# Kernel optimization log

Measured on AMD Instinct MI355X. Metric: run time of the kernel, lower is better.

## Reference

```python
import jax, jax.numpy as jnp
import numpy as np

N = 100000  # nodes
E = 600000  # edges (avg degree ~6, mesh-like)
HID = 128


def _lin(key, fan_in, fan_out):
    # torch Linear default init: U(-1/sqrt(fan_in), 1/sqrt(fan_in))
    bound = 1.0 / np.sqrt(fan_in)
    return jax.random.uniform(key, (fan_in, fan_out), jnp.float32, -bound, bound)


def setup_inputs() -> dict:
    key = jax.random.key(0)
    ks = jax.random.split(key, 8)
    x = jax.random.normal(ks[0], (N, 3), jnp.float32)
    edge_index = jax.random.randint(ks[1], (2, E), 0, N, dtype=jnp.int32)
    return {
        "x": x,
        "edge_index": edge_index,
        "W1": _lin(ks[2], 3, HID),          "b1": jnp.zeros((HID,), jnp.float32),
        "W2": _lin(ks[3], HID, HID),        "b2": jnp.zeros((HID,), jnp.float32),
        "W3": _lin(ks[4], HID, HID // 2),   "b3": jnp.zeros((HID // 2,), jnp.float32),
        "W4": _lin(ks[5], HID // 2, HID // 2), "b4": jnp.zeros((HID // 2,), jnp.float32),
        "W5": _lin(ks[6], HID // 2, 1),     "b5": jnp.zeros((1,), jnp.float32),
    }


def reference(x, edge_index, W1, b1, W2, b2, W3, b3, W4, b4, W5, b5):
    n = x.shape[0]
    # add self loops (same graph used by every layer)
    loops = jnp.arange(n, dtype=edge_index.dtype)
    row = jnp.concatenate([edge_index[0], loops])  # sources (x_j index)
    col = jnp.concatenate([edge_index[1], loops])  # targets (aggregation index)
    # symmetric degree normalization: norm_e = d[row]^-0.5 * d[col]^-0.5
    deg = jax.ops.segment_sum(jnp.ones(col.shape, x.dtype), col, num_segments=n)
    dis = jnp.where(deg > 0, deg ** -0.5, 0.0)
    norm = (dis[row] * dis[col])[:, None]  # [E+N, 1]

    def conv(h, W, b):
        h = h @ W                                   # [N, out]
        msg = norm * h[row]                         # gather + scale  [E+N, out]
        return jax.ops.segment_sum(msg, col, num_segments=n) + b  # scatter-add

    h = jax.nn.relu(conv(x, W1, b1))
    h = jax.nn.relu(conv(h, W2, b2))
    h = jax.nn.relu(conv(h, W3, b3))
    h = jax.nn.relu(conv(h, W4, b4))
    return conv(h, W5, b5)  # [N, 1]
```

## Files before the change

kernel.cpp:

```cpp
#include <hip/hip_runtime.h>
#include <hip/hip_bf16.h>
#include <stdint.h>


#define NB 256
#define CAP 64

typedef __attribute__((ext_vector_type(8))) short bf16x8;
typedef __attribute__((ext_vector_type(4))) float f32x4;

static __host__ __device__ inline int ceil_div(int a, int b) { return (a + b - 1) / b; }

__device__ inline ushort f32_to_bf16(float x) {
    uint32_t u = __float_as_uint(x);
    uint32_t r = (u + 0x7fffu + ((u >> 16) & 1u)) >> 16;
    return (ushort)r;
}
__device__ inline float bf16_lo(uint32_t u) { return __uint_as_float(u << 16); }
__device__ inline float bf16_hi(uint32_t u) { return __uint_as_float(u & 0xffff0000u); }


template <int K, int F>
__device__ inline void pack_one(const float* __restrict__ W, ushort* __restrict__ Wp, int id) {
    constexpr int KS = K / 32;
    int j = id & 7;
    int lane = (id >> 3) & 63;
    int ts = id >> 9;
    int s = ts % KS;
    int t = ts / KS;
    int k = s * 32 + ((lane >> 4) << 3) + j;
    int f = t * 16 + (lane & 15);
    Wp[id] = f32_to_bf16(W[k * F + f]);
}

__global__ void k_init(int* __restrict__ cursor, int n, int zero_blocks,
                       const float* __restrict__ W2, const float* __restrict__ W3,
                       const float* __restrict__ W4, ushort* __restrict__ Wp2,
                       ushort* __restrict__ Wp3, ushort* __restrict__ Wp4) {
    int b = blockIdx.x;
    if (b < zero_blocks) {
        int i = b * NB + threadIdx.x;
        if (i < n) cursor[i] = 0;
    } else {
        int id = (b - zero_blocks) * NB + threadIdx.x;
        if (id < 16384) pack_one<128, 128>(W2, Wp2, id);
        else if (id < 24576) pack_one<128, 64>(W3, Wp3, id - 16384);
        else if (id < 28672) pack_one<64, 64>(W4, Wp4, id - 24576);
    }
}


__global__ void k_fillb(const int* __restrict__ row, const int* __restrict__ col, int e,
                        int* __restrict__ cursor, int* __restrict__ bucket) {
    int T = (e + 7) >> 3;
    int t = blockIdx.x * NB + threadIdx.x;
    int i[8];
#pragma unroll
    for (int k = 0; k < 8; ++k) i[k] = t + k * T;
    if (i[7] < e) {
        int c[8], r[8], s[8];
#pragma unroll
        for (int k = 0; k < 8; ++k) { c[k] = col[i[k]]; r[k] = row[i[k]]; }
#pragma unroll
        for (int k = 0; k < 8; ++k) s[k] = atomicAdd(&cursor[c[k]], 1);
#pragma unroll
        for (int k = 0; k < 8; ++k) bucket[(size_t)c[k] * CAP + s[k]] = r[k];
    } else {
#pragma unroll
        for (int k = 0; k < 8; ++k) {
            if (i[k] < e) {
                int c = col[i[k]], r = row[i[k]];
                int s = atomicAdd(&cursor[c], 1);
                bucket[(size_t)c * CAP + s] = r;
            }
        }
    }
}

__global__ void k_dis(const int* __restrict__ cnt, const float* __restrict__ x,
                      float* __restrict__ dis, float4* __restrict__ xs4,
                      int* __restrict__ bucket, ushort* __restrict__ A,
                      ushort* __restrict__ B, ushort* __restrict__ C,
                      float* __restrict__ zbuf, int n) {
    int i = blockIdx.x * NB + threadIdx.x;
    if (i < n) {
        int deg = cnt[i];
        float d = rsqrtf((float)(deg + 1));
        dis[i] = d;
        xs4[i] = make_float4(d * x[3 * i], d * x[3 * i + 1], d * x[3 * i + 2], 0.f);
        int dp = (deg + 3) & ~3;
        for (int e = deg; e < dp; ++e) bucket[(size_t)i * CAP + e] = n;
    } else if (i == n) {
        xs4[n] = make_float4(0.f, 0.f, 0.f, 0.f);
        zbuf[n] = 0.f;
        uint4 z = make_uint4(0, 0, 0, 0);
        uint4* Bn = (uint4*)(B + (size_t)n * 128);
        uint4* An = (uint4*)(A + (size_t)n * 64);
        uint4* Cn = (uint4*)(C + (size_t)n * 64);
#pragma unroll
        for (int k = 0; k < 16; ++k) Bn[k] = z;
#pragma unroll
        for (int k = 0; k < 8; ++k) { An[k] = z; Cn[k] = z; }
    }
}


__global__ __launch_bounds__(256) void k_l1mm(const float4* __restrict__ xs4,
                                              const int* __restrict__ cnt,
                                              const int* __restrict__ bucket,
                                              const float* __restrict__ dis,
                                              const float* __restrict__ W1,
                                              const float* __restrict__ b1,
                                              const ushort* __restrict__ Wp2,
                                              ushort* __restrict__ Zout, int n) {
    __shared__ float w[512];
    __shared__ float s_a[64][4];
    __shared__ ushort tileH[64][136];
    for (int t = threadIdx.x; t < 512; t += 256)
        w[t] = (t < 384) ? W1[t] : b1[t - 384];

    int node0 = blockIdx.x * 64;
    int local = threadIdx.x >> 2;
    int sub = threadIdx.x & 3;
    int i = node0 + local;
    float a0 = 0.f, a1 = 0.f, a2 = 0.f;
    if (i < n) {
        if (sub == 0) {
            float4 self = xs4[i];
            a0 = self.x; a1 = self.y; a2 = self.z;
        }
        int deg = cnt[i];
        const int* bk = bucket + (size_t)i * CAP;
        for (int e = sub; e < deg; e += 4) {
            float4 v = xs4[bk[e]];
            a0 += v.x; a1 += v.y; a2 += v.z;
        }
    }
    a0 += __shfl_xor(a0, 1, 64); a1 += __shfl_xor(a1, 1, 64); a2 += __shfl_xor(a2, 1, 64);
    a0 += __shfl_xor(a0, 2, 64); a1 += __shfl_xor(a1, 2, 64); a2 += __shfl_xor(a2, 2, 64);
    if (sub == 0) {
        float d = (i < n) ? dis[i] : 0.f;
        s_a[local][0] = a0 * d;
        s_a[local][1] = a1 * d;
        s_a[local][2] = a2 * d;
    }
    __syncthreads();

#pragma unroll
    for (int it = 0; it < 16; ++it) {
        int id = it * 256 + threadIdx.x;
        int lc = id >> 6;
        int f = (id & 63) * 2;
        float h0 = s_a[lc][0], h1 = s_a[lc][1], h2 = s_a[lc][2];
        float v0 = fmaxf(h0 * w[f] + h1 * w[128 + f] + h2 * w[256 + f] + w[384 + f], 0.f);
        float v1 = fmaxf(h0 * w[f + 1] + h1 * w[128 + f + 1] + h2 * w[256 + f + 1] + w[384 + f + 1], 0.f);
        *(uint32_t*)&tileH[lc][f] = ((uint32_t)f32_to_bf16(v1) << 16) | (uint32_t)f32_to_bf16(v0);
    }
    __syncthreads();

    constexpr int KS = 4, FT = 8;
    int wid = threadIdx.x >> 6;
    int lane = threadIdx.x & 63;
    int m = lane & 15;
    int quad = lane >> 4;
    int tbase = wid * 16;
    bf16x8 a[KS];
#pragma unroll
    for (int s = 0; s < KS; ++s)
        a[s] = *(const bf16x8*)&tileH[tbase + m][s * 32 + quad * 8];
    float dsc[4];
#pragma unroll
    for (int r = 0; r < 4; ++r) {
        int node = node0 + tbase + quad * 4 + r;
        dsc[r] = (node < n) ? dis[node] : 0.f;
    }
    const bf16x8* bp = (const bf16x8*)Wp2;
#pragma unroll
    for (int t = 0; t < FT; ++t) {
        f32x4 acc = {0.f, 0.f, 0.f, 0.f};
#pragma unroll
        for (int s = 0; s < KS; ++s)
            acc = __builtin_amdgcn_mfma_f32_16x16x32_bf16(a[s], bp[(t * KS + s) * 64 + lane], acc, 0, 0, 0);
        int feat = t * 16 + m;
#pragma unroll
        for (int r = 0; r < 4; ++r) {
            int node = node0 + tbase + quad * 4 + r;
            if (node < n) Zout[(size_t)node * 128 + feat] = f32_to_bf16(acc[r] * dsc[r]);
        }
    }
}


__device__ inline void add8(float (&a)[8], uint4 v) {
    a[0] += bf16_lo(v.x);
    a[1] += bf16_hi(v.x);
    a[2] += bf16_lo(v.y);
    a[3] += bf16_hi(v.y);
    a[4] += bf16_lo(v.z);
    a[5] += bf16_hi(v.z);
    a[6] += bf16_lo(v.w);
    a[7] += bf16_hi(v.w);
}

template <int L>
__device__ inline void agg_sum(float (&a)[8], const uint4* __restrict__ Zq,
                               const int* __restrict__ bk, int degp, int l, int i) {
    add8(a, Zq[(size_t)i * L + l]);
    for (int e = 0; e < degp; e += 4) {
        int4 j4 = *(const int4*)(bk + e);
        uint4 v0 = Zq[(size_t)j4.x * L + l];
        uint4 v1 = Zq[(size_t)j4.y * L + l];
        uint4 v2 = Zq[(size_t)j4.z * L + l];
        uint4 v3 = Zq[(size_t)j4.w * L + l];
        add8(a, v0);
        add8(a, v1);
        add8(a, v2);
        add8(a, v3);
    }
}

__device__ inline uint4 pack8s(const float (&a)[8], float d, const float* __restrict__ bias, int l) {
    float4 b0 = *(const float4*)&bias[8 * l];
    float4 b1 = *(const float4*)&bias[8 * l + 4];
    float r0 = fmaxf(a[0] * d + b0.x, 0.f), r1 = fmaxf(a[1] * d + b0.y, 0.f);
    float r2 = fmaxf(a[2] * d + b0.z, 0.f), r3 = fmaxf(a[3] * d + b0.w, 0.f);
    float r4 = fmaxf(a[4] * d + b1.x, 0.f), r5 = fmaxf(a[5] * d + b1.y, 0.f);
    float r6 = fmaxf(a[6] * d + b1.z, 0.f), r7 = fmaxf(a[7] * d + b1.w, 0.f);
    uint4 o;
    o.x = ((uint32_t)f32_to_bf16(r1) << 16) | (uint32_t)f32_to_bf16(r0);
    o.y = ((uint32_t)f32_to_bf16(r3) << 16) | (uint32_t)f32_to_bf16(r2);
    o.z = ((uint32_t)f32_to_bf16(r5) << 16) | (uint32_t)f32_to_bf16(r4);
    o.w = ((uint32_t)f32_to_bf16(r7) << 16) | (uint32_t)f32_to_bf16(r6);
    return o;
}


template <int FIN, int FOUT>
__global__ __launch_bounds__(256) void k_aggmm(const ushort* __restrict__ Zin,
                                               const float* __restrict__ bias,
                                               const int* __restrict__ cnt,
                                               const int* __restrict__ bucket,
                                               const float* __restrict__ dis,
                                               const ushort* __restrict__ Wp,
                                               ushort* __restrict__ Zout, int n) {
    constexpr int L = FIN / 8;
    constexpr int GROUPS = 256 / L;
    constexpr int PASSES = 64 / GROUPS;
    __shared__ ushort tileA[64][FIN + 8];
    int node0 = blockIdx.x * 64;

    {
        int l = threadIdx.x & (L - 1);
        int g = threadIdx.x / L;
#pragma unroll
        for (int pass = 0; pass < PASSES; ++pass) {
            int local = pass * GROUPS + g;
            int i = node0 + local;
            if (i < n) {
                float a[8] = {0.f, 0.f, 0.f, 0.f, 0.f, 0.f, 0.f, 0.f};
                int degp = (cnt[i] + 3) & ~3;
                agg_sum<L>(a, (const uint4*)Zin, bucket + (size_t)i * CAP, degp, l, i);
                *(uint4*)&tileA[local][l * 8] = pack8s(a, dis[i], bias, l);
            }
        }
    }
    __syncthreads();

    constexpr int KS = FIN / 32;
    constexpr int FT = FOUT / 16;
    int wid = threadIdx.x >> 6;
    int lane = threadIdx.x & 63;
    int m = lane & 15;
    int quad = lane >> 4;
    int tbase = wid * 16;
    bf16x8 a[KS];
#pragma unroll
    for (int s = 0; s < KS; ++s)
        a[s] = *(const bf16x8*)&tileA[tbase + m][s * 32 + quad * 8];
    float dsc[4];
#pragma unroll
    for (int r = 0; r < 4; ++r) {
        int node = node0 + tbase + quad * 4 + r;
        dsc[r] = (node < n) ? dis[node] : 0.f;
    }
    const bf16x8* bp = (const bf16x8*)Wp;
#pragma unroll
    for (int t = 0; t < FT; ++t) {
        f32x4 acc = {0.f, 0.f, 0.f, 0.f};
#pragma unroll
        for (int s = 0; s < KS; ++s)
            acc = __builtin_amdgcn_mfma_f32_16x16x32_bf16(a[s], bp[(t * KS + s) * 64 + lane], acc, 0, 0, 0);
        int feat = t * 16 + m;
#pragma unroll
        for (int r = 0; r < 4; ++r) {
            int node = node0 + tbase + quad * 4 + r;
            if (node < n) Zout[(size_t)node * FOUT + feat] = f32_to_bf16(acc[r] * dsc[r]);
        }
    }
}

__global__ __launch_bounds__(256) void k_agg64z(const ushort* __restrict__ Z,
                                                const float* __restrict__ bias,
                                                const float* __restrict__ W5,
                                                const int* __restrict__ cnt,
                                                const int* __restrict__ bucket,
                                                const float* __restrict__ dis,
                                                float* __restrict__ zbuf, int n) {
    int l = threadIdx.x & 7;
    int i = blockIdx.x * 32 + (threadIdx.x >> 3);
    if (i >= n) return;
    float a[8] = {0.f, 0.f, 0.f, 0.f, 0.f, 0.f, 0.f, 0.f};
    int degp = (cnt[i] + 3) & ~3;
    agg_sum<8>(a, (const uint4*)Z, bucket + (size_t)i * CAP, degp, l, i);
    float d = dis[i];
    float4 b0 = *(const float4*)&bias[8 * l];
    float4 b1 = *(const float4*)&bias[8 * l + 4];
    float4 w0 = *(const float4*)&W5[8 * l];
    float4 w1 = *(const float4*)&W5[8 * l + 4];
    float p = fmaxf(a[0] * d + b0.x, 0.f) * w0.x + fmaxf(a[1] * d + b0.y, 0.f) * w0.y +
              fmaxf(a[2] * d + b0.z, 0.f) * w0.z + fmaxf(a[3] * d + b0.w, 0.f) * w0.w +
              fmaxf(a[4] * d + b1.x, 0.f) * w1.x + fmaxf(a[5] * d + b1.y, 0.f) * w1.y +
              fmaxf(a[6] * d + b1.z, 0.f) * w1.z + fmaxf(a[7] * d + b1.w, 0.f) * w1.w;
#pragma unroll
    for (int off = 4; off; off >>= 1) p += __shfl_xor(p, off, 64);
    if (l == 0) zbuf[i] = d * p;
}

__global__ void k_agg1(const float* __restrict__ zbuf, const float* __restrict__ b5,
                       const int* __restrict__ cnt, const int* __restrict__ bucket,
                       const float* __restrict__ dis, float* __restrict__ out, int n) {
    int i = blockIdx.x * NB + threadIdx.x;
    if (i >= n) return;
    float acc = zbuf[i];
    int degp = (cnt[i] + 3) & ~3;
    const int* bk = bucket + (size_t)i * CAP;
    for (int e = 0; e < degp; e += 4) {
        int4 j4 = *(const int4*)(bk + e);
        acc += zbuf[j4.x] + zbuf[j4.y] + zbuf[j4.z] + zbuf[j4.w];
    }
    out[i] = dis[i] * acc + b5[0];
}


static inline size_t align_up(size_t x) { return (x + 255) & ~(size_t)255; }

extern "C" void kernel_launch(void* const* d_in, const int* in_sizes, int n_in,
                              void* d_out, int out_size, void* d_ws, size_t ws_size,
                              hipStream_t stream) {
    const int n = in_sizes[0] / 3;
    const int e = in_sizes[1] / 2;

    const float* x   = (const float*)d_in[0];
    const int*   ei  = (const int*)d_in[1];
    const int*   row = ei;
    const int*   col = ei + e;
    const float* W1 = (const float*)d_in[2];  const float* b1 = (const float*)d_in[3];
    const float* W2 = (const float*)d_in[4];  const float* b2 = (const float*)d_in[5];
    const float* W3 = (const float*)d_in[6];  const float* b3 = (const float*)d_in[7];
    const float* W4 = (const float*)d_in[8];  const float* b4 = (const float*)d_in[9];
    const float* W5 = (const float*)d_in[10]; const float* b5 = (const float*)d_in[11];
    float* out = (float*)d_out;

    char* base = (char*)d_ws;
    size_t off = 0;
    auto alloc = [&](size_t bytes) { char* p = base + off; off = align_up(off + bytes); return p; };
    int*    cursor = (int*)alloc((size_t)n * 4);
    float*  dis    = (float*)alloc((size_t)n * 4);
    float4* xs4    = (float4*)alloc((size_t)(n + 1) * 16);
    int*    bucket = (int*)alloc((size_t)n * CAP * 4);
    ushort* A      = (ushort*)alloc((size_t)(n + 1) * 64 * 2);
    ushort* B      = (ushort*)alloc((size_t)(n + 1) * 128 * 2);
    ushort* C      = (ushort*)alloc((size_t)(n + 1) * 64 * 2);
    float*  zbuf   = (float*)alloc((size_t)(n + 1) * 4);
    ushort* Wp2    = (ushort*)alloc(128 * 128 * 2);
    ushort* Wp3    = (ushort*)alloc(128 * 64 * 2);
    ushort* Wp4    = (ushort*)alloc(64 * 64 * 2);
    (void)ws_size;

    const int gn = ceil_div(n, NB);
    const int pack_blocks = ceil_div(16384 + 8192 + 4096, NB);

    k_init<<<gn + pack_blocks, NB, 0, stream>>>(cursor, n, gn, W2, W3, W4, Wp2, Wp3, Wp4);
    k_fillb<<<ceil_div(ceil_div(e, 8), NB), NB, 0, stream>>>(row, col, e, cursor, bucket);
    k_dis<<<gn, NB, 0, stream>>>(cursor, x, dis, xs4, bucket, A, B, C, zbuf, n);

    k_l1mm<<<ceil_div(n, 64), 256, 0, stream>>>(xs4, cursor, bucket, dis, W1, b1, Wp2, B, n);

    k_aggmm<128, 64><<<ceil_div(n, 64), 256, 0, stream>>>(B, b2, cursor, bucket, dis, Wp3, A, n);

    k_aggmm<64, 64><<<ceil_div(n, 64), 256, 0, stream>>>(A, b3, cursor, bucket, dis, Wp4, C, n);

    k_agg64z<<<ceil_div(n, 32), 256, 0, stream>>>(C, b4, W5, cursor, bucket, dis, zbuf, n);

    k_agg1<<<gn, NB, 0, stream>>>(zbuf, b5, cursor, bucket, dis, out, n);
}
```

Baseline: 213.5 us.

## Aggregate layer-2 input before matmul using 8-bit quantized layer-1 activations

Layer 2 now aggregates the 128-wide layer-1 activations first and applies W2 afterwards (A·H·W = (A·H)·W). The W2 and W3 matmuls are fused into one kernel, so the bf16 B intermediate is gone. The gathered activations are stored as per-node 8-bit unsigned values with a float scale, halving gather bytes compared with bf16. Bucket padding is widened to multiples of 8 for an 8-way unrolled gather loop. This cuts memory traffic in the gather-heavy layer but adds quantization error on the layer-1 activations, which could hurt accuracy against tolerance.

```diff
diff --git a/kernel.cpp b/kernel.cpp
--- a/kernel.cpp
+++ b/kernel.cpp
@@ -79,43 +79,41 @@
 
 __global__ void k_dis(const int* __restrict__ cnt, const float* __restrict__ x,
                       float* __restrict__ dis, float4* __restrict__ xs4,
-                      int* __restrict__ bucket, ushort* __restrict__ A,
-                      ushort* __restrict__ B, ushort* __restrict__ C,
-                      float* __restrict__ zbuf, int n) {
+                      int* __restrict__ bucket, uint8_t* __restrict__ G,
+                      float* __restrict__ sG, ushort* __restrict__ A,
+                      ushort* __restrict__ C, float* __restrict__ zbuf, int n) {
     int i = blockIdx.x * NB + threadIdx.x;
     if (i < n) {
         int deg = cnt[i];
         float d = rsqrtf((float)(deg + 1));
         dis[i] = d;
         xs4[i] = make_float4(d * x[3 * i], d * x[3 * i + 1], d * x[3 * i + 2], 0.f);
-        int dp = (deg + 3) & ~3;
+        int dp = (deg + 7) & ~7;
         for (int e = deg; e < dp; ++e) bucket[(size_t)i * CAP + e] = n;
     } else if (i == n) {
         xs4[n] = make_float4(0.f, 0.f, 0.f, 0.f);
         zbuf[n] = 0.f;
+        sG[n] = 0.f;
         uint4 z = make_uint4(0, 0, 0, 0);
-        uint4* Bn = (uint4*)(B + (size_t)n * 128);
+        uint4* Gn = (uint4*)(G + (size_t)n * 128);
         uint4* An = (uint4*)(A + (size_t)n * 64);
         uint4* Cn = (uint4*)(C + (size_t)n * 64);
 #pragma unroll
-        for (int k = 0; k < 16; ++k) Bn[k] = z;
-#pragma unroll
-        for (int k = 0; k < 8; ++k) { An[k] = z; Cn[k] = z; }
-    }
-}
-
-
-__global__ __launch_bounds__(256) void k_l1mm(const float4* __restrict__ xs4,
-                                              const int* __restrict__ cnt,
-                                              const int* __restrict__ bucket,
-                                              const float* __restrict__ dis,
-                                              const float* __restrict__ W1,
-                                              const float* __restrict__ b1,
-                                              const ushort* __restrict__ Wp2,
-                                              ushort* __restrict__ Zout, int n) {
+        for (int k = 0; k < 8; ++k) { Gn[k] = z; An[k] = z; Cn[k] = z; }
+    }
+}
+
+
+__global__ __launch_bounds__(256) void k_l1q(const float4* __restrict__ xs4,
+                                             const int* __restrict__ cnt,
+                                             const int* __restrict__ bucket,
+                                             const float* __restrict__ dis,
+                                             const float* __restrict__ W1,
+                                             const float* __restrict__ b1,
+                                             uint8_t* __restrict__ G,
+                                             float* __restrict__ sG, int n) {
     __shared__ float w[512];
     __shared__ float s_a[64][4];
-    __shared__ ushort tileH[64][136];
     for (int t = threadIdx.x; t < 512; t += 256)
         w[t] = (t < 384) ? W1[t] : b1[t - 384];
 
@@ -143,6 +141,7 @@
         s_a[local][0] = a0 * d;
         s_a[local][1] = a1 * d;
         s_a[local][2] = a2 * d;
+        s_a[local][3] = d;
     }
     __syncthreads();
 
@@ -151,41 +150,140 @@
         int id = it * 256 + threadIdx.x;
         int lc = id >> 6;
         int f = (id & 63) * 2;
-        float h0 = s_a[lc][0], h1 = s_a[lc][1], h2 = s_a[lc][2];
-        float v0 = fmaxf(h0 * w[f] + h1 * w[128 + f] + h2 * w[256 + f] + w[384 + f], 0.f);
-        float v1 = fmaxf(h0 * w[f + 1] + h1 * w[128 + f + 1] + h2 * w[256 + f + 1] + w[384 + f + 1], 0.f);
-        *(uint32_t*)&tileH[lc][f] = ((uint32_t)f32_to_bf16(v1) << 16) | (uint32_t)f32_to_bf16(v0);
+        float h0 = s_a[lc][0], h1 = s_a[lc][1], h2 = s_a[lc][2], d = s_a[lc][3];
+        float v0 = fmaxf(h0 * w[f] + h1 * w[128 + f] + h2 * w[256 + f] + w[384 + f], 0.f) * d;
+        float v1 = fmaxf(h0 * w[f + 1] + h1 * w[128 + f + 1] + h2 * w[256 + f + 1] + w[384 + f + 1], 0.f) * d;
+        float m = fmaxf(v0, v1);
+#pragma unroll
+        for (int off = 1; off < 64; off <<= 1) m = fmaxf(m, __shfl_xor(m, off, 64));
+        float inv = (m > 0.f) ? 255.f / m : 0.f;
+        uint32_t u0 = (uint32_t)__float2int_rn(v0 * inv);
+        uint32_t u1 = (uint32_t)__float2int_rn(v1 * inv);
+        int node = node0 + lc;
+        if (node < n) {
+            *(ushort*)&G[(size_t)node * 128 + f] = (ushort)(u0 | (u1 << 8));
+            if ((threadIdx.x & 63) == 0) sG[node] = m * (1.f / 255.f);
+        }
+    }
+}
+
+
+__device__ inline void accum_u8(float (&a)[8], uint2 v, float s) {
+    uint32_t x = v.x, y = v.y;
+    a[0] = fmaf((float)(x & 0xffu), s, a[0]);
+    a[1] = fmaf((float)((x >> 8) & 0xffu), s, a[1]);
+    a[2] = fmaf((float)((x >> 16) & 0xffu), s, a[2]);
+    a[3] = fmaf((float)(x >> 24), s, a[3]);
+    a[4] = fmaf((float)(y & 0xffu), s, a[4]);
+    a[5] = fmaf((float)((y >> 8) & 0xffu), s, a[5]);
+    a[6] = fmaf((float)((y >> 16) & 0xffu), s, a[6]);
+    a[7] = fmaf((float)(y >> 24), s, a[7]);
+}
+
+__global__ __launch_bounds__(256) void k_aggu8(const uint8_t* __restrict__ G,
+                                               const float* __restrict__ sG,
+                                               const float* __restrict__ b2,
+                                               const int* __restrict__ cnt,
+                                               const int* __restrict__ bucket,
+                                               const float* __restrict__ dis,
+                                               const ushort* __restrict__ Wp2,
+                                               const ushort* __restrict__ Wp3,
+                                               ushort* __restrict__ A, int n) {
+    __shared__ ushort tile[64][136];
+    int node0 = blockIdx.x * 64;
+    const uint2* Gq = (const uint2*)G;
+
+    {
+        int l = threadIdx.x & 15;
+        int g = threadIdx.x >> 4;
+#pragma unroll
+        for (int pass = 0; pass < 4; ++pass) {
+            int local = pass * 16 + g;
+            int i = node0 + local;
+            if (i < n) {
+                float a[8] = {0.f, 0.f, 0.f, 0.f, 0.f, 0.f, 0.f, 0.f};
+                int degp = (cnt[i] + 7) & ~7;
+                const int* bk = bucket + (size_t)i * CAP;
+                accum_u8(a, Gq[(size_t)i * 16 + l], sG[i]);
+                for (int e = 0; e < degp; e += 8) {
+                    int4 ja = *(const int4*)(bk + e);
+                    int4 jb = *(const int4*)(bk + e + 4);
+                    uint2 v0 = Gq[(size_t)ja.x * 16 + l]; float s0 = sG[ja.x];
+                    uint2 v1 = Gq[(size_t)ja.y * 16 + l]; float s1 = sG[ja.y];
+                    uint2 v2 = Gq[(size_t)ja.z * 16 + l]; float s2 = sG[ja.z];
+                    uint2 v3 = Gq[(size_t)ja.w * 16 + l]; float s3 = sG[ja.w];
+                    uint2 v4 = Gq[(size_t)jb.x * 16 + l]; float s4 = sG[jb.x];
+                    uint2 v5 = Gq[(size_t)jb.y * 16 + l]; float s5 = sG[jb.y];
+                    uint2 v6 = Gq[(size_t)jb.z * 16 + l]; float s6 = sG[jb.z];
+                    uint2 v7 = Gq[(size_t)jb.w * 16 + l]; float s7 = sG[jb.w];
+                    accum_u8(a, v0, s0);
+                    accum_u8(a, v1, s1);
+                    accum_u8(a, v2, s2);
+                    accum_u8(a, v3, s3);
+                    accum_u8(a, v4, s4);
+                    accum_u8(a, v5, s5);
+                    accum_u8(a, v6, s6);
+                    accum_u8(a, v7, s7);
+                }
+                float d = dis[i];
+                uint4 o;
+                o.x = ((uint32_t)f32_to_bf16(d * a[1]) << 16) | (uint32_t)f32_to_bf16(d * a[0]);
+                o.y = ((uint32_t)f32_to_bf16(d * a[3]) << 16) | (uint32_t)f32_to_bf16(d * a[2]);
+                o.z = ((uint32_t)f32_to_bf16(d * a[5]) << 16) | (uint32_t)f32_to_bf16(d * a[4]);
+                o.w = ((uint32_t)f32_to_bf16(d * a[7]) << 16) | (uint32_t)f32_to_bf16(d * a[6]);
+                *(uint4*)&tile[local][l * 8] = o;
+            }
+        }
     }
     __syncthreads();
 
-    constexpr int KS = 4, FT = 8;
     int wid = threadIdx.x >> 6;
     int lane = threadIdx.x & 63;
     int m = lane & 15;
     int quad = lane >> 4;
     int tbase = wid * 16;
-    bf16x8 a[KS];
-#pragma unroll
-    for (int s = 0; s < KS; ++s)
-        a[s] = *(const bf16x8*)&tileH[tbase + m][s * 32 + quad * 8];
+
+    bf16x8 af[4];
+#pragma unroll
+    for (int s = 0; s < 4; ++s)
+        af[s] = *(const bf16x8*)&tile[tbase + m][s * 32 + quad * 8];
+    float b2v[8];
+#pragma unroll
+    for (int t = 0; t < 8; ++t) b2v[t] = b2[t * 16 + m];
+    const bf16x8* bp2 = (const bf16x8*)Wp2;
+#pragma unroll
+    for (int t = 0; t < 8; ++t) {
+        f32x4 acc = {0.f, 0.f, 0.f, 0.f};
+#pragma unroll
+        for (int s = 0; s < 4; ++s)
+            acc = __builtin_amdgcn_mfma_f32_16x16x32_bf16(af[s], bp2[(t * 4 + s) * 64 + lane], acc, 0, 0, 0);
+#pragma unroll
+        for (int r = 0; r < 4; ++r)
+            tile[tbase + quad * 4 + r][t * 16 + m] = f32_to_bf16(fmaxf(acc[r] + b2v[t], 0.f));
+    }
+
+    bf16x8 af2[4];
+#pragma unroll
+    for (int s = 0; s < 4; ++s)
+        af2[s] = *(const bf16x8*)&tile[tbase + m][s * 32 + quad * 8];
     float dsc[4];
 #pragma unroll
     for (int r = 0; r < 4; ++r) {
         int node = node0 + tbase + quad * 4 + r;
         dsc[r] = (node < n) ? dis[node] : 0.f;
     }
-    const bf16x8* bp = (const bf16x8*)Wp2;
-#pragma unroll
-    for (int t = 0; t < FT; ++t) {
+    const bf16x8* bp3 = (const bf16x8*)Wp3;
+#pragma unroll
+    for (int t = 0; t < 4; ++t) {
         f32x4 acc = {0.f, 0.f, 0.f, 0.f};
 #pragma unroll
-        for (int s = 0; s < KS; ++s)
-            acc = __builtin_amdgcn_mfma_f32_16x16x32_bf16(a[s], bp[(t * KS + s) * 64 + lane], acc, 0, 0, 0);
+        for (int s = 0; s < 4; ++s)
+            acc = __builtin_amdgcn_mfma_f32_16x16x32_bf16(af2[s], bp3[(t * 4 + s) * 64 + lane], acc, 0, 0, 0);
         int feat = t * 16 + m;
 #pragma unroll
         for (int r = 0; r < 4; ++r) {
             int node = node0 + tbase + quad * 4 + r;
-            if (node < n) Zout[(size_t)node * 128 + feat] = f32_to_bf16(acc[r] * dsc[r]);
+            if (node < n) A[(size_t)node * 64 + feat] = f32_to_bf16(acc[r] * dsc[r]);
         }
     }
 }
@@ -364,17 +462,18 @@
     char* base = (char*)d_ws;
     size_t off = 0;
     auto alloc = [&](size_t bytes) { char* p = base + off; off = align_up(off + bytes); return p; };
-    int*    cursor = (int*)alloc((size_t)n * 4);
-    float*  dis    = (float*)alloc((size_t)n * 4);
-    float4* xs4    = (float4*)alloc((size_t)(n + 1) * 16);
-    int*    bucket = (int*)alloc((size_t)n * CAP * 4);
-    ushort* A      = (ushort*)alloc((size_t)(n + 1) * 64 * 2);
-    ushort* B      = (ushort*)alloc((size_t)(n + 1) * 128 * 2);
-    ushort* C      = (ushort*)alloc((size_t)(n + 1) * 64 * 2);
-    float*  zbuf   = (float*)alloc((size_t)(n + 1) * 4);
-    ushort* Wp2    = (ushort*)alloc(128 * 128 * 2);
-    ushort* Wp3    = (ushort*)alloc(128 * 64 * 2);
-    ushort* Wp4    = (ushort*)alloc(64 * 64 * 2);
+    int*     cursor = (int*)alloc((size_t)n * 4);
+    float*   dis    = (float*)alloc((size_t)n * 4);
+    float4*  xs4    = (float4*)alloc((size_t)(n + 1) * 16);
+    int*     bucket = (int*)alloc((size_t)n * CAP * 4);
+    uint8_t* G      = (uint8_t*)alloc((size_t)(n + 1) * 128);
+    float*   sG     = (float*)alloc((size_t)(n + 1) * 4);
+    ushort*  A      = (ushort*)alloc((size_t)(n + 1) * 64 * 2);
+    ushort*  C      = (ushort*)alloc((size_t)(n + 1) * 64 * 2);
+    float*   zbuf   = (float*)alloc((size_t)(n + 1) * 4);
+    ushort*  Wp2    = (ushort*)alloc(128 * 128 * 2);
+    ushort*  Wp3    = (ushort*)alloc(128 * 64 * 2);
+    ushort*  Wp4    = (ushort*)alloc(64 * 64 * 2);
     (void)ws_size;
 
     const int gn = ceil_div(n, NB);
@@ -382,11 +481,11 @@
 
     k_init<<<gn + pack_blocks, NB, 0, stream>>>(cursor, n, gn, W2, W3, W4, Wp2, Wp3, Wp4);
     k_fillb<<<ceil_div(ceil_div(e, 8), NB), NB, 0, stream>>>(row, col, e, cursor, bucket);
-    k_dis<<<gn, NB, 0, stream>>>(cursor, x, dis, xs4, bucket, A, B, C, zbuf, n);
-
-    k_l1mm<<<ceil_div(n, 64), 256, 0, stream>>>(xs4, cursor, bucket, dis, W1, b1, Wp2, B, n);
-
-    k_aggmm<128, 64><<<ceil_div(n, 64), 256, 0, stream>>>(B, b2, cursor, bucket, dis, Wp3, A, n);
+    k_dis<<<gn, NB, 0, stream>>>(cursor, x, dis, xs4, bucket, G, sG, A, C, zbuf, n);
+
+    k_l1q<<<ceil_div(n, 64), 256, 0, stream>>>(xs4, cursor, bucket, dis, W1, b1, G, sG, n);
+
+    k_aggu8<<<ceil_div(n, 64), 256, 0, stream>>>(G, sG, b2, cursor, bucket, dis, Wp2, Wp3, A, n);
 
     k_aggmm<64, 64><<<ceil_div(n, 64), 256, 0, stream>>>(A, b3, cursor, bucket, dis, Wp4, C, n);
 
```

Result: no change. 216.2 us (+1.2%).
